# Performance work log

Measured on AMD Instinct MI355X. Metric: run time of the kernel, lower is better.

The kernel has to match this reference:

```python
import jax, jax.numpy as jnp
import numpy as np

N, K, D = 16384, 32, 256
NEG_SLOPE = 0.01  # torch F.leaky_relu default


def setup_inputs() -> dict:
    key = jax.random.key(0)
    k1, k2, k3, k4 = jax.random.split(key, 4)
    scale = 1.0 / np.sqrt(D)
    return {
        "target": jax.random.normal(k1, (N, D), dtype=jnp.float32),
        "middle": jax.random.normal(k2, (N, K, D), dtype=jnp.float32),
        "W": jax.random.normal(k3, (D, D), dtype=jnp.float32) * scale,
        "b": jnp.zeros((D,), dtype=jnp.float32),
        "a_w": jax.random.normal(k4, (1, D), dtype=jnp.float32) * scale,
        "a_b": jnp.zeros((1,), dtype=jnp.float32),
    }


def reference(target, middle, W, b, a_w, a_b):
    # attention_weight applied to both target and middle (bias added to each,
    # matching the torch code which sums two Linear outputs)
    pt = target @ W.T + b              # [N, D]
    pm = middle @ W.T + b              # [N, K, D]
    h = pt[:, None, :] + pm            # [N, K, D]
    # a_weight: D -> 1
    score = h @ a_w.T + a_b            # [N, K, 1]
    score = jax.nn.leaky_relu(score, negative_slope=NEG_SLOPE)
    coef = jax.nn.softmax(score, axis=-2)   # softmax over neighbor dim K
    neighbor_feature = jnp.sum(coef * middle, axis=-2)  # [N, D]
    return neighbor_feature
```

## Files before the change

### kernel.cpp

```cpp
#include <hip/hip_runtime.h>

#define N_ 16384
#define K_ 32
#define D_ 256
#define NEG_SLOPE 0.01f

__global__ __launch_bounds__(256) void prep_kernel(
    const float* __restrict__ W, const float* __restrict__ b,
    const float* __restrict__ a_w, const float* __restrict__ a_b,
    float* __restrict__ ws) {
  const int t = threadIdx.x;
  const int i = blockIdx.x;
  float acc = 0.f;
#pragma unroll
  for (int j = 0; j < 8; ++j) {
    const int d = i * 8 + j;
    acc += a_w[d] * W[d * D_ + t];
  }
  atomicAdd(&ws[t], acc);

  if (i == 0) {
    float s = b[t] * a_w[t];
#pragma unroll
    for (int off = 1; off < 64; off <<= 1) s += __shfl_xor(s, off);
    __shared__ float sp[4];
    if ((t & 63) == 0) sp[t >> 6] = s;
    __syncthreads();
    if (t == 0)
      atomicAdd(&ws[D_], 2.f * (sp[0] + sp[1] + sp[2] + sp[3]) + a_b[0]);
  }
}

__global__ __launch_bounds__(512, 8) void attn_agg_kernel(
    const float* __restrict__ target, const float* __restrict__ middle,
    const float* __restrict__ ws, float* __restrict__ out) {
  __shared__ __align__(16) float part[8][D_];
  __shared__ float sdot[K_];
  __shared__ float scoef[K_];
  __shared__ float stp[4];

  const int t = threadIdx.x;
  const int kg = t >> 6;
  const int l = t & 63;
  const int n = blockIdx.x;

  const float4* m4p = (const float4*)(middle + (size_t)n * K_ * D_);
  float4 m[4];
#pragma unroll
  for (int j = 0; j < 4; ++j) m[j] = m4p[(kg * 4 + j) * 64 + l];

  const float4 vv = ((const float4*)ws)[l];
  const float cadd = ws[D_];

  float pd[4];
#pragma unroll
  for (int j = 0; j < 4; ++j)
    pd[j] = m[j].x * vv.x + m[j].y * vv.y + m[j].z * vv.z + m[j].w * vv.w;

#pragma unroll
  for (int j = 0; j < 4; ++j) pd[j] += __shfl_xor(pd[j], 32);
  float q0 = (l & 32) ? pd[2] : pd[0];
  float q1 = (l & 32) ? pd[3] : pd[1];
  q0 += __shfl_xor(q0, 16);
  q1 += __shfl_xor(q1, 16);
  float r = (l & 16) ? q1 : q0;
  r += __shfl_xor(r, 8);
  r += __shfl_xor(r, 4);
  r += __shfl_xor(r, 2);
  r += __shfl_xor(r, 1);
  if ((l & 15) == 0)
    sdot[kg * 4 + ((l >> 5) * 2 + ((l >> 4) & 1))] = r;

  if (t < D_) {
    float tp = target[(size_t)n * D_ + t] * ws[t];
#pragma unroll
    for (int off = 1; off < 64; off <<= 1) tp += __shfl_xor(tp, off);
    if (l == 0) stp[kg] = tp;
  }
  __syncthreads();

  if (t < 64) {
    const float tdot = stp[0] + stp[1] + stp[2] + stp[3];
    const int k = t & 31;
    float sc = sdot[k] + tdot + cadd;
    sc = sc > 0.f ? sc : NEG_SLOPE * sc;
    float mx = sc;
    mx = fmaxf(mx, __shfl_xor(mx, 1));
    mx = fmaxf(mx, __shfl_xor(mx, 2));
    mx = fmaxf(mx, __shfl_xor(mx, 4));
    mx = fmaxf(mx, __shfl_xor(mx, 8));
    mx = fmaxf(mx, __shfl_xor(mx, 16));
    float ex = __expf(sc - mx);
    float sum = ex;
    sum += __shfl_xor(sum, 1);
    sum += __shfl_xor(sum, 2);
    sum += __shfl_xor(sum, 4);
    sum += __shfl_xor(sum, 8);
    sum += __shfl_xor(sum, 16);
    if (t < 32) scoef[k] = ex / sum;
  }
  __syncthreads();

  float4 acc = make_float4(0.f, 0.f, 0.f, 0.f);
#pragma unroll
  for (int j = 0; j < 4; ++j) {
    const float cf = scoef[kg * 4 + j];
    acc.x += cf * m[j].x;
    acc.y += cf * m[j].y;
    acc.z += cf * m[j].z;
    acc.w += cf * m[j].w;
  }
  *(float4*)(&part[kg][4 * l]) = acc;
  __syncthreads();

  if (t < D_) {
    float o = 0.f;
#pragma unroll
    for (int w = 0; w < 8; ++w) o += part[w][t];
    out[(size_t)n * D_ + t] = o;
  }
}

extern "C" void kernel_launch(void* const* d_in, const int* in_sizes, int n_in,
                              void* d_out, int out_size, void* d_ws, size_t ws_size,
                              hipStream_t stream) {
  const float* target = (const float*)d_in[0];
  const float* middle = (const float*)d_in[1];
  const float* W      = (const float*)d_in[2];
  const float* b      = (const float*)d_in[3];
  const float* a_w    = (const float*)d_in[4];
  const float* a_b    = (const float*)d_in[5];
  float* out = (float*)d_out;
  float* ws  = (float*)d_ws;

  hipMemsetAsync(ws, 0, (D_ + 1) * sizeof(float), stream);
  prep_kernel<<<32, 256, 0, stream>>>(W, b, a_w, a_b, ws);
  attn_agg_kernel<<<N_, 512, 0, stream>>>(target, middle, ws, out);
}
```

Measured before the change: 110.8 us.

## Assign one wavefront per row and keep all neighbor vectors in registers

The aggregation kernel now gives each 64-lane wavefront a whole output row and loads all 32 neighbor float4 vectors into registers. The 32 dot products are reduced with a staged shuffle-and-select tree, the softmax runs in-wave, and the coefficients are broadcast with readlane. This removes shared memory, every __syncthreads, and the cross-wave partial-sum pass. The cost is about 128+ VGPRs per thread under launch_bounds(256,2), which lowers occupancy. The kernel is near the memory-bandwidth limit, so the gain may be small.

```diff
diff --git a/kernel.cpp b/kernel.cpp
--- a/kernel.cpp
+++ b/kernel.cpp
@@ -31,94 +31,91 @@
   }
 }
 
-__global__ __launch_bounds__(512, 8) void attn_agg_kernel(
+__global__ __launch_bounds__(256, 2) void attn_agg_kernel(
     const float* __restrict__ target, const float* __restrict__ middle,
     const float* __restrict__ ws, float* __restrict__ out) {
-  __shared__ __align__(16) float part[8][D_];
-  __shared__ float sdot[K_];
-  __shared__ float scoef[K_];
-  __shared__ float stp[4];
-
   const int t = threadIdx.x;
-  const int kg = t >> 6;
+  const int w = t >> 6;
   const int l = t & 63;
-  const int n = blockIdx.x;
+  const int n = blockIdx.x * 4 + w;
 
   const float4* m4p = (const float4*)(middle + (size_t)n * K_ * D_);
-  float4 m[4];
-#pragma unroll
-  for (int j = 0; j < 4; ++j) m[j] = m4p[(kg * 4 + j) * 64 + l];
-
   const float4 vv = ((const float4*)ws)[l];
   const float cadd = ws[D_];
+  const float4 tg = ((const float4*)(target + (size_t)n * D_))[l];
 
-  float pd[4];
+  float4 m[K_];
 #pragma unroll
-  for (int j = 0; j < 4; ++j)
-    pd[j] = m[j].x * vv.x + m[j].y * vv.y + m[j].z * vv.z + m[j].w * vv.w;
+  for (int j = 0; j < K_; ++j) m[j] = m4p[j * 64 + l];
 
+  float pd[16];
 #pragma unroll
-  for (int j = 0; j < 4; ++j) pd[j] += __shfl_xor(pd[j], 32);
-  float q0 = (l & 32) ? pd[2] : pd[0];
-  float q1 = (l & 32) ? pd[3] : pd[1];
-  q0 += __shfl_xor(q0, 16);
-  q1 += __shfl_xor(q1, 16);
-  float r = (l & 16) ? q1 : q0;
-  r += __shfl_xor(r, 8);
-  r += __shfl_xor(r, 4);
-  r += __shfl_xor(r, 2);
-  r += __shfl_xor(r, 1);
-  if ((l & 15) == 0)
-    sdot[kg * 4 + ((l >> 5) * 2 + ((l >> 4) & 1))] = r;
+  for (int j = 0; j < 16; ++j) {
+    float d = m[j].x * vv.x + m[j].y * vv.y + m[j].z * vv.z + m[j].w * vv.w;
+    d += __shfl_xor(d, 32);
+    pd[j] = d;
+  }
+#pragma unroll
+  for (int j = 16; j < 32; ++j) {
+    float d = m[j].x * vv.x + m[j].y * vv.y + m[j].z * vv.z + m[j].w * vv.w;
+    d += __shfl_xor(d, 32);
+    pd[j - 16] = (l & 32) ? d : pd[j - 16];
+  }
+#pragma unroll
+  for (int i = 0; i < 16; ++i) pd[i] += __shfl_xor(pd[i], 16);
+#pragma unroll
+  for (int i = 0; i < 8; ++i) pd[i] = (l & 16) ? pd[i + 8] : pd[i];
+#pragma unroll
+  for (int i = 0; i < 8; ++i) pd[i] += __shfl_xor(pd[i], 8);
+#pragma unroll
+  for (int i = 0; i < 4; ++i) pd[i] = (l & 8) ? pd[i + 4] : pd[i];
+#pragma unroll
+  for (int i = 0; i < 4; ++i) pd[i] += __shfl_xor(pd[i], 4);
+#pragma unroll
+  for (int i = 0; i < 2; ++i) pd[i] = (l & 4) ? pd[i + 2] : pd[i];
+#pragma unroll
+  for (int i = 0; i < 2; ++i) pd[i] += __shfl_xor(pd[i], 2);
+  pd[0] = (l & 2) ? pd[1] : pd[0];
+  pd[0] += __shfl_xor(pd[0], 1);
 
-  if (t < D_) {
-    float tp = target[(size_t)n * D_ + t] * ws[t];
-#pragma unroll
-    for (int off = 1; off < 64; off <<= 1) tp += __shfl_xor(tp, off);
-    if (l == 0) stp[kg] = tp;
-  }
-  __syncthreads();
+  float tp = tg.x * vv.x + tg.y * vv.y + tg.z * vv.z + tg.w * vv.w;
+  tp += __shfl_xor(tp, 32);
+  tp += __shfl_xor(tp, 16);
+  tp += __shfl_xor(tp, 8);
+  tp += __shfl_xor(tp, 4);
+  tp += __shfl_xor(tp, 2);
+  tp += __shfl_xor(tp, 1);
 
-  if (t < 64) {
-    const float tdot = stp[0] + stp[1] + stp[2] + stp[3];
-    const int k = t & 31;
-    float sc = sdot[k] + tdot + cadd;
-    sc = sc > 0.f ? sc : NEG_SLOPE * sc;
-    float mx = sc;
-    mx = fmaxf(mx, __shfl_xor(mx, 1));
-    mx = fmaxf(mx, __shfl_xor(mx, 2));
-    mx = fmaxf(mx, __shfl_xor(mx, 4));
-    mx = fmaxf(mx, __shfl_xor(mx, 8));
-    mx = fmaxf(mx, __shfl_xor(mx, 16));
-    float ex = __expf(sc - mx);
-    float sum = ex;
-    sum += __shfl_xor(sum, 1);
-    sum += __shfl_xor(sum, 2);
-    sum += __shfl_xor(sum, 4);
-    sum += __shfl_xor(sum, 8);
-    sum += __shfl_xor(sum, 16);
-    if (t < 32) scoef[k] = ex / sum;
-  }
-  __syncthreads();
+  float sc = pd[0] + tp + cadd;
+  sc = sc > 0.f ? sc : NEG_SLOPE * sc;
+  float mx = sc;
+  mx = fmaxf(mx, __shfl_xor(mx, 32));
+  mx = fmaxf(mx, __shfl_xor(mx, 16));
+  mx = fmaxf(mx, __shfl_xor(mx, 8));
+  mx = fmaxf(mx, __shfl_xor(mx, 4));
+  mx = fmaxf(mx, __shfl_xor(mx, 2));
+  mx = fmaxf(mx, __shfl_xor(mx, 1));
+  const float ex = __expf(sc - mx);
+  float sm = ex;
+  sm += __shfl_xor(sm, 32);
+  sm += __shfl_xor(sm, 16);
+  sm += __shfl_xor(sm, 8);
+  sm += __shfl_xor(sm, 4);
+  sm += __shfl_xor(sm, 2);
+  sm += __shfl_xor(sm, 1);
+  const float coef = 2.f * ex / sm;
 
   float4 acc = make_float4(0.f, 0.f, 0.f, 0.f);
 #pragma unroll
-  for (int j = 0; j < 4; ++j) {
-    const float cf = scoef[kg * 4 + j];
+  for (int j = 0; j < K_; ++j) {
+    const float cf =
+        __int_as_float(__builtin_amdgcn_readlane(__float_as_int(coef), 2 * j));
     acc.x += cf * m[j].x;
     acc.y += cf * m[j].y;
     acc.z += cf * m[j].z;
     acc.w += cf * m[j].w;
   }
-  *(float4*)(&part[kg][4 * l]) = acc;
-  __syncthreads();
-
-  if (t < D_) {
-    float o = 0.f;
-#pragma unroll
-    for (int w = 0; w < 8; ++w) o += part[w][t];
-    out[(size_t)n * D_ + t] = o;
-  }
+  ((float4*)(out + (size_t)n * D_))[l] = acc;
 }
 
 extern "C" void kernel_launch(void* const* d_in, const int* in_sizes, int n_in,
@@ -135,5 +132,5 @@
 
   hipMemsetAsync(ws, 0, (D_ + 1) * sizeof(float), stream);
   prep_kernel<<<32, 256, 0, stream>>>(W, b, a_w, a_b, ws);
-  attn_agg_kernel<<<N_, 512, 0, stream>>>(target, middle, ws, out);
+  attn_agg_kernel<<<N_ / 4, 256, 0, stream>>>(target, middle, ws, out);
 }
```

Measured after the change: 127.0 us. +14.7%, slower.

## Drop memset and atomics in prep; compute softmax redundantly per wave

Applied to the files above, without the earlier changes.

The prep kernel now runs as a single 1024-thread block that reduces through shared memory and writes the workspace directly, so the memset launch and the atomics are gone. In the main kernel every wave computes the 32-way softmax itself and reads its coefficients with readlane, which removes one block-wide barrier and the shared coefficient buffer. The final reduction now uses 64 threads with float4 loads and stores. The trade-off is redundant exp and shuffle work in all eight waves, plus a single-block prep kernel that reads all of W serially.

```diff
diff --git a/kernel.cpp b/kernel.cpp
--- a/kernel.cpp
+++ b/kernel.cpp
@@ -5,30 +5,32 @@
 #define D_ 256
 #define NEG_SLOPE 0.01f
 
-__global__ __launch_bounds__(256) void prep_kernel(
+__global__ __launch_bounds__(1024) void prep_kernel(
     const float* __restrict__ W, const float* __restrict__ b,
     const float* __restrict__ a_w, const float* __restrict__ a_b,
     float* __restrict__ ws) {
+  __shared__ float part[4][D_];
+  __shared__ float sp[4];
   const int t = threadIdx.x;
-  const int i = blockIdx.x;
+  const int dd = t >> 8;
+  const int e = t & 255;
   float acc = 0.f;
-#pragma unroll
-  for (int j = 0; j < 8; ++j) {
-    const int d = i * 8 + j;
-    acc += a_w[d] * W[d * D_ + t];
+#pragma unroll 8
+  for (int j = 0; j < 64; ++j) {
+    const int d = dd * 64 + j;
+    acc += a_w[d] * W[d * D_ + e];
   }
-  atomicAdd(&ws[t], acc);
+  part[dd][e] = acc;
 
-  if (i == 0) {
+  if (t < D_) {
     float s = b[t] * a_w[t];
 #pragma unroll
     for (int off = 1; off < 64; off <<= 1) s += __shfl_xor(s, off);
-    __shared__ float sp[4];
     if ((t & 63) == 0) sp[t >> 6] = s;
-    __syncthreads();
-    if (t == 0)
-      atomicAdd(&ws[D_], 2.f * (sp[0] + sp[1] + sp[2] + sp[3]) + a_b[0]);
   }
+  __syncthreads();
+  if (t < D_) ws[t] = part[0][t] + part[1][t] + part[2][t] + part[3][t];
+  if (t == 0) ws[D_] = 2.f * (sp[0] + sp[1] + sp[2] + sp[3]) + a_b[0];
 }
 
 __global__ __launch_bounds__(512, 8) void attn_agg_kernel(
@@ -36,7 +38,6 @@
     const float* __restrict__ ws, float* __restrict__ out) {
   __shared__ __align__(16) float part[8][D_];
   __shared__ float sdot[K_];
-  __shared__ float scoef[K_];
   __shared__ float stp[4];
 
   const int t = threadIdx.x;
@@ -56,7 +57,6 @@
 #pragma unroll
   for (int j = 0; j < 4; ++j)
     pd[j] = m[j].x * vv.x + m[j].y * vv.y + m[j].z * vv.z + m[j].w * vv.w;
-
 #pragma unroll
   for (int j = 0; j < 4; ++j) pd[j] += __shfl_xor(pd[j], 32);
   float q0 = (l & 32) ? pd[2] : pd[0];
@@ -79,32 +79,29 @@
   }
   __syncthreads();
 
-  if (t < 64) {
-    const float tdot = stp[0] + stp[1] + stp[2] + stp[3];
-    const int k = t & 31;
-    float sc = sdot[k] + tdot + cadd;
-    sc = sc > 0.f ? sc : NEG_SLOPE * sc;
-    float mx = sc;
-    mx = fmaxf(mx, __shfl_xor(mx, 1));
-    mx = fmaxf(mx, __shfl_xor(mx, 2));
-    mx = fmaxf(mx, __shfl_xor(mx, 4));
-    mx = fmaxf(mx, __shfl_xor(mx, 8));
-    mx = fmaxf(mx, __shfl_xor(mx, 16));
-    float ex = __expf(sc - mx);
-    float sum = ex;
-    sum += __shfl_xor(sum, 1);
-    sum += __shfl_xor(sum, 2);
-    sum += __shfl_xor(sum, 4);
-    sum += __shfl_xor(sum, 8);
-    sum += __shfl_xor(sum, 16);
-    if (t < 32) scoef[k] = ex / sum;
-  }
-  __syncthreads();
+  const float tdot = stp[0] + stp[1] + stp[2] + stp[3];
+  float sc = sdot[l & 31] + tdot + cadd;
+  sc = sc > 0.f ? sc : NEG_SLOPE * sc;
+  float mx = sc;
+  mx = fmaxf(mx, __shfl_xor(mx, 1));
+  mx = fmaxf(mx, __shfl_xor(mx, 2));
+  mx = fmaxf(mx, __shfl_xor(mx, 4));
+  mx = fmaxf(mx, __shfl_xor(mx, 8));
+  mx = fmaxf(mx, __shfl_xor(mx, 16));
+  const float ex = __expf(sc - mx);
+  float sm = ex;
+  sm += __shfl_xor(sm, 1);
+  sm += __shfl_xor(sm, 2);
+  sm += __shfl_xor(sm, 4);
+  sm += __shfl_xor(sm, 8);
+  sm += __shfl_xor(sm, 16);
+  const float coef = ex / sm;
 
   float4 acc = make_float4(0.f, 0.f, 0.f, 0.f);
 #pragma unroll
   for (int j = 0; j < 4; ++j) {
-    const float cf = scoef[kg * 4 + j];
+    const float cf = __int_as_float(
+        __builtin_amdgcn_readlane(__float_as_int(coef), kg * 4 + j));
     acc.x += cf * m[j].x;
     acc.y += cf * m[j].y;
     acc.z += cf * m[j].z;
@@ -113,11 +110,14 @@
   *(float4*)(&part[kg][4 * l]) = acc;
   __syncthreads();
 
-  if (t < D_) {
-    float o = 0.f;
+  if (t < 64) {
+    float4 o = make_float4(0.f, 0.f, 0.f, 0.f);
 #pragma unroll
-    for (int w = 0; w < 8; ++w) o += part[w][t];
-    out[(size_t)n * D_ + t] = o;
+    for (int w = 0; w < 8; ++w) {
+      const float4 p = *(const float4*)(&part[w][4 * t]);
+      o.x += p.x; o.y += p.y; o.z += p.z; o.w += p.w;
+    }
+    ((float4*)(out + (size_t)n * D_))[t] = o;
   }
 }
 
@@ -133,7 +133,6 @@
   float* out = (float*)d_out;
   float* ws  = (float*)d_ws;
 
-  hipMemsetAsync(ws, 0, (D_ + 1) * sizeof(float), stream);
-  prep_kernel<<<32, 256, 0, stream>>>(W, b, a_w, a_b, ws);
+  prep_kernel<<<1, 1024, 0, stream>>>(W, b, a_w, a_b, ws);
   attn_agg_kernel<<<N_, 512, 0, stream>>>(target, middle, ws, out);
 }
```

Result: faster. 108.4 us, median of 2 (-2.1%).
